# Kernel tuning notes

Measured on AMD Instinct MI355X. Metric: run time of the kernel, lower is better.

The kernel has to match this reference:

```python
import jax, jax.numpy as jnp
import numpy as np

EMBED_DIM = 1024
N_HEADS = 16

def setup_inputs() -> dict:
    key = jax.random.key(0)
    ks = jax.random.split(key, 5)
    C = EMBED_DIM
    std = 1.0 / np.sqrt(C)
    x = jax.random.normal(ks[0], (2, 2048, C), dtype=jnp.float32)
    w_attn = jax.random.normal(ks[1], (C, 3 * C), dtype=jnp.float32) * std  # (in, out)
    b_attn = jax.random.normal(ks[2], (3 * C,), dtype=jnp.float32) * 0.01
    w_proj = jax.random.normal(ks[3], (C, C), dtype=jnp.float32) * std
    b_proj = jax.random.normal(ks[4], (C,), dtype=jnp.float32) * 0.01
    return {"x": x, "w_attn": w_attn, "b_attn": b_attn, "w_proj": w_proj, "b_proj": b_proj}

def reference(x, w_attn, b_attn, w_proj, b_proj):
    B, T, C = x.shape
    H = N_HEADS
    D = C // H
    qkv = x @ w_attn + b_attn                      # (B, T, 3C)
    q, k, v = jnp.split(qkv, 3, axis=2)
    # (B, T, C) -> (B, H, T, D)
    q = q.reshape(B, T, H, D).transpose(0, 2, 1, 3)
    k = k.reshape(B, T, H, D).transpose(0, 2, 1, 3)
    v = v.reshape(B, T, H, D).transpose(0, 2, 1, 3)
    # Faithful to source: query is divided by scale BEFORE QK^T, and the
    # similarity is divided by scale AGAIN before softmax (net scale = 1/D).
    scale = jnp.asarray(D, dtype=x.dtype) ** 0.5
    q = q / scale
    sim = jnp.einsum('bhnd,bhsd->bhns', q, k)      # (B, H, T, T)
    causal = jnp.tril(jnp.ones((T, T), dtype=bool))
    neg_min = jnp.finfo(sim.dtype).min
    sim = jnp.where(causal[None, None, :, :], sim, neg_min)
    attn = jax.nn.softmax(sim / scale, axis=-1)
    out = jnp.einsum('bhns,bhsd->bhnd', attn, v)   # (B, H, T, D)
    # source: gqa returns (b n h d), forward does transpose(1,2) -> (b h n d)
    # then .view(B, T, C); net effect is reshaping the (B,H,T,D) layout.
    y = out.reshape(B, T, C)
    y = y @ w_proj + b_proj
    return y
```

## Files before the change

kernel.cpp:

```cpp
#include <hip/hip_runtime.h>
#include <hip/hip_bf16.h>

#define BB 2
#define TT 2048
#define CC 1024
#define HH 16
#define DD 64
#define MM (BB*TT)
#define QSZ ((size_t)MM*CC)

#define QSCALE 0.022542110013890053f

typedef __attribute__((ext_vector_type(8))) short bf16x8;
typedef __attribute__((ext_vector_type(4))) float f32x4;
typedef __attribute__((address_space(1))) const unsigned char as1_u8;
typedef __attribute__((address_space(3))) unsigned char as3_u8;

struct alignas(8) bf16x4_s { __hip_bfloat16 h[4]; };

static __device__ __forceinline__ unsigned cvt_pk_bf16(float lo, float hi) {
    unsigned r;
    asm("v_cvt_pk_bf16_f32 %0, %1, %2" : "=v"(r) : "v"(lo), "v"(hi));
    return r;
}

static __device__ __forceinline__ float fast_exp2(float x) {
    return __builtin_amdgcn_exp2f(x);
}

__constant__ unsigned char U_sqi[30] = {
    5,11,11,10,10,15,15, 4,9,9,13,14,14,14,15, 8,8,12,12,13,13,
    3,7,7,12, 6,6, 2,1,0};
__constant__ unsigned char U_t0[30] = {
    0,0,12,0,11,0,11, 0,0,10,0,0,10,20,22, 0,9,0,9,10,19,
    0,0,8,18, 0,7, 0,0,0};
__constant__ unsigned char U_t1[30] = {
    12,12,24,11,22,11,22, 10,10,20,10,10,20,30,32, 9,18,9,18,19,28,
    8,8,16,26, 7,14, 6,4,2};
__constant__ unsigned char U_pu[30] = {
    255,10,11,8,9,21,22, 255,6,7,15,18,19,20,23, 4,5,12,13,16,17,
    255,2,3,14, 0,1, 255,255,255};

__global__ __launch_bounds__(256) void prep_kernel(
    const float* __restrict__ x,  __hip_bfloat16* __restrict__ xb,
    const float* __restrict__ wa, __hip_bfloat16* __restrict__ wqkvT,
    const float* __restrict__ wp, __hip_bfloat16* __restrict__ wprojT)
{
    __shared__ float tile[64][68];
    const int t = threadIdx.x;
    const int b = blockIdx.x;
    if (b < 2048) {
        const int i = (b * 256 + t) * 8;
        const float4 a = *(const float4*)&x[i];
        const float4 c = *(const float4*)&x[i + 4];
        uint2 lo, hi;
        lo.x = cvt_pk_bf16(a.x, a.y); lo.y = cvt_pk_bf16(a.z, a.w);
        hi.x = cvt_pk_bf16(c.x, c.y); hi.y = cvt_pk_bf16(c.z, c.w);
        *(uint2*)&xb[i] = lo;
        *(uint2*)&xb[i + 4] = hi;
        return;
    }
    const float* in; __hip_bfloat16* outp; int R, Cc, bx, by;
    if (b < 2816) { const int i = b - 2048; in = wa; outp = wqkvT; R = CC; Cc = 3*CC; bx = i % 48; by = i / 48; }
    else          { const int i = b - 2816; in = wp; outp = wprojT; R = CC; Cc = CC;  bx = i % 16; by = i / 16; }
    const int c0 = bx * 64, r0 = by * 64;
    {
        const int r = t >> 2, cb = (t & 3) * 16;
        #pragma unroll
        for (int i = 0; i < 4; ++i)
            *(float4*)&tile[r][cb + i*4] = *(const float4*)&in[(size_t)(r0 + r)*Cc + c0 + cb + i*4];
    }
    __syncthreads();
    {
        const int c = t >> 2, rb = (t & 3) * 16;
        uint2 o0, o1;
        o0.x = cvt_pk_bf16(tile[rb+0][c],  tile[rb+1][c]);
        o0.y = cvt_pk_bf16(tile[rb+2][c],  tile[rb+3][c]);
        o1.x = cvt_pk_bf16(tile[rb+4][c],  tile[rb+5][c]);
        o1.y = cvt_pk_bf16(tile[rb+6][c],  tile[rb+7][c]);
        __hip_bfloat16* dst = outp + (size_t)(c0 + c)*R + r0 + rb;
        *(uint2*)&dst[0] = o0; *(uint2*)&dst[4] = o1;
        o0.x = cvt_pk_bf16(tile[rb+8][c],  tile[rb+9][c]);
        o0.y = cvt_pk_bf16(tile[rb+10][c], tile[rb+11][c]);
        o1.x = cvt_pk_bf16(tile[rb+12][c], tile[rb+13][c]);
        o1.y = cvt_pk_bf16(tile[rb+14][c], tile[rb+15][c]);
        *(uint2*)&dst[8] = o0; *(uint2*)&dst[12] = o1;
    }
}

template<int MODE>
__global__ __launch_bounds__(256) void gemm_mfma(
    const __hip_bfloat16* __restrict__ A,
    const __hip_bfloat16* __restrict__ BT,
    const float* __restrict__ bias,
    void* __restrict__ out, int M, int N, int K)
{
    __shared__ __hip_bfloat16 As[128][64];
    __shared__ __hip_bfloat16 Bs[128][64];

    const int tid = threadIdx.x;
    const int w = tid >> 6, l = tid & 63;
    const int lr = l & 15, lg = l >> 4;
    const int wr = w >> 1, wc = w & 1;
    const int rsw = (lr & 7) << 4;
    const int lsw = ((l & 7) ^ (l >> 3)) * 8;

    const int nwg = gridDim.x * gridDim.y;
    const int bid = blockIdx.y * gridDim.x + blockIdx.x;
    const int swz_id = (bid & 7) * (nwg >> 3) + (bid >> 3);
    const int row0 = (swz_id / gridDim.x) * 128;
    const int col0 = (swz_id % gridDim.x) * 128;

    f32x4 acc[4][4] = {};

    for (int k0 = 0; k0 < K; k0 += 64) {
        __syncthreads();
        #pragma unroll
        for (int i = 0; i < 4; ++i) {
            const int br = w*32 + i*8;
            const __hip_bfloat16* ga = A  + (size_t)(row0 + br + (l>>3))*K + k0 + lsw;
            __builtin_amdgcn_global_load_lds((as1_u8*)ga, (as3_u8*)&As[br][0], 16, 0, 0);
            const __hip_bfloat16* gb = BT + (size_t)(col0 + br + (l>>3))*K + k0 + lsw;
            __builtin_amdgcn_global_load_lds((as1_u8*)gb, (as3_u8*)&Bs[br][0], 16, 0, 0);
        }
        __syncthreads();

        #pragma unroll
        for (int s = 0; s < 2; ++s) {
            bf16x8 af[4], bfr[4];
            #pragma unroll
            for (int m = 0; m < 4; ++m) {
                const char* ab = (const char*)&As[wr*64 + m*16 + lr][0];
                af[m] = *(const bf16x8*)(ab + ((s*64 + lg*16) ^ rsw));
            }
            #pragma unroll
            for (int n = 0; n < 4; ++n) {
                const char* bb = (const char*)&Bs[wc*64 + n*16 + lr][0];
                bfr[n] = *(const bf16x8*)(bb + ((s*64 + lg*16) ^ rsw));
            }
            #pragma unroll
            for (int m = 0; m < 4; ++m)
                #pragma unroll
                for (int n = 0; n < 4; ++n)
                    acc[m][n] = __builtin_amdgcn_mfma_f32_16x16x32_bf16(af[m], bfr[n], acc[m][n], 0, 0, 0);
        }
    }

    #pragma unroll
    for (int m = 0; m < 4; ++m) {
        #pragma unroll
        for (int n = 0; n < 4; ++n) {
            const int ng = col0 + wc*64 + n*16 + lr;
            const float bv = bias[ng];
            const int mg0 = row0 + wr*64 + m*16 + lg*4;
            if (MODE == 0) {
                const int which = ng >> 10, c = ng & 1023;
                const int h = c >> 6, d = c & 63;
                if (which == 2) {
                    const int b = mg0 >> 11, t0 = mg0 & 2047;
                    uint2 pv;
                    pv.x = cvt_pk_bf16(acc[m][n][0] + bv, acc[m][n][1] + bv);
                    pv.y = cvt_pk_bf16(acc[m][n][2] + bv, acc[m][n][3] + bv);
                    *(uint2*)((__hip_bfloat16*)out + (size_t)2*QSZ +
                        (((size_t)(b*HH + h))*DD + d)*TT + t0) = pv;
                } else {
                    #pragma unroll
                    for (int r = 0; r < 4; ++r) {
                        const int mg = mg0 + r;
                        float v = acc[m][n][r] + bv;
                        if (which == 0) v *= QSCALE;
                        const int b = mg >> 11, t = mg & 2047;
                        ((__hip_bfloat16*)out)[(size_t)which*QSZ +
                            (((size_t)(b*HH + h))*TT + t)*DD + d] = __float2bfloat16(v);
                    }
                }
            } else {
                #pragma unroll
                for (int r = 0; r < 4; ++r)
                    ((float*)out)[(size_t)(mg0 + r)*N + ng] = acc[m][n][r] + bv;
            }
        }
    }
}

__global__ __launch_bounds__(512) void attn_mfma(
    const __hip_bfloat16* __restrict__ Qb,
    const __hip_bfloat16* __restrict__ Kb,
    const __hip_bfloat16* __restrict__ Vb,
    __hip_bfloat16* __restrict__ Ob,
    __hip_bfloat16* __restrict__ Opart,
    float* __restrict__ Lpart)
{
    __shared__ __hip_bfloat16 k_lds[64][64];
    __shared__ __hip_bfloat16 vT[64][64];
    __shared__ __hip_bfloat16 p_lds[8][16][64];

    const int tid = threadIdx.x;
    const int w  = tid >> 6;
    const int l  = tid & 63;
    const int lr = l & 15;
    const int lg = l >> 4;
    const int swz = (lr & 7) << 4;

    const int bid  = blockIdx.x;
    const int loc  = bid >> 3;
    const int bh   = (bid & 7) * 4 + (loc & 3);
    const int u    = loc >> 2;
    const int sqi  = U_sqi[u];
    const int t0i  = U_t0[u];
    const int t1i  = U_t1[u];
    const int pu   = U_pu[u];
    const int qb   = sqi * 128;

    const __hip_bfloat16* Qh = Qb + (size_t)bh*TT*DD;
    const __hip_bfloat16* Kh = Kb + (size_t)bh*TT*DD;
    const __hip_bfloat16* Vh = Vb + (size_t)bh*DD*TT;

    bf16x8 qa[2];
    const int qrow = qb + w*16 + lr;
    {
        const __hip_bfloat16* qp = Qh + (size_t)qrow*DD + lg*8;
        qa[0] = *(const bf16x8*)(qp);
        qa[1] = *(const bf16x8*)(qp + 32);
    }

    const int off0 = (16*lg) ^ swz;
    const int off1 = (64 + 16*lg) ^ swz;
    const char* kr0b = (const char*)&k_lds[lr][0];
    const char* vr0b = (const char*)&vT[lr][0];
    char* pwb = (char*)&p_lds[w][lr][0];
    int pwo[4];
    #pragma unroll
    for (int mt = 0; mt < 4; ++mt) pwo[mt] = (32*mt + 8*lg) ^ swz;

    const int sthalf = tid >> 8;
    const int stid = tid & 255;
    const int srow = stid >> 2, sch = stid & 3;
    const int wswz = (srow & 7) << 4;
    char* swr = sthalf ? (char*)&vT[srow][0] : (char*)&k_lds[srow][0];
    const int wo0 = (sch*32) ^ wswz, wo1 = (sch*32 + 16) ^ wswz;
    const __hip_bfloat16* ssrc = sthalf
        ? (Vh + (size_t)srow*TT + t0i*64 + sch*16)
        : (Kh + (size_t)(t0i*64 + srow)*DD + sch*16);
    const size_t sstride = sthalf ? 64 : (size_t)64*DD;

    float4 sr0 = *(const float4*)ssrc, sr1 = *(const float4*)(ssrc + 8);
    ssrc += sstride;
    *(float4*)(swr + wo0) = sr0; *(float4*)(swr + wo1) = sr1;
    __syncthreads();

    f32x4 oacc[4] = {};
    f32x4 lacc = {0.f, 0.f, 0.f, 0.f};

    for (int t = t0i; t < t1i; ++t) {
        const int kv0 = t * 64;
        const bool has_next = (t + 1 < t1i);

        if (has_next) {
            sr0 = *(const float4*)ssrc; sr1 = *(const float4*)(ssrc + 8);
            ssrc += sstride;
        }

        const bool dead = (w < 4) && (t == 2*sqi + 1);
        if (!dead) {
            f32x4 sacc[4] = {};
            __builtin_amdgcn_s_setprio(1);
            #pragma unroll
            for (int mt = 0; mt < 4; ++mt) {
                const bf16x8 kb0 = *(const bf16x8*)(kr0b + mt*2048 + off0);
                const bf16x8 kb1 = *(const bf16x8*)(kr0b + mt*2048 + off1);
                sacc[mt] = __builtin_amdgcn_mfma_f32_16x16x32_bf16(kb0, qa[0], sacc[mt], 0, 0, 0);
                sacc[mt] = __builtin_amdgcn_mfma_f32_16x16x32_bf16(kb1, qa[1], sacc[mt], 0, 0, 0);
            }
            __builtin_amdgcn_s_setprio(0);

            if (t >= 2*sqi) {
                #pragma unroll
                for (int mt = 0; mt < 4; ++mt)
                    #pragma unroll
                    for (int r = 0; r < 4; ++r)
                        if (kv0 + mt*16 + lg*4 + r > qrow) sacc[mt][r] = -3.0e38f;
            }
            #pragma unroll
            for (int mt = 0; mt < 4; ++mt) {
                const float p0 = fast_exp2(sacc[mt][0]), p1 = fast_exp2(sacc[mt][1]);
                const float p2 = fast_exp2(sacc[mt][2]), p3 = fast_exp2(sacc[mt][3]);
                lacc[mt] += (p0 + p1) + (p2 + p3);
                uint2 pp;
                pp.x = cvt_pk_bf16(p0, p1);
                pp.y = cvt_pk_bf16(p2, p3);
                *(uint2*)(pwb + pwo[mt]) = pp;
            }

            const bf16x8 pb0 = *(const bf16x8*)(pwb + off0);
            const bf16x8 pb1 = *(const bf16x8*)(pwb + off1);
            __builtin_amdgcn_s_setprio(1);
            #pragma unroll
            for (int dt = 0; dt < 4; ++dt) {
                const bf16x8 vb0 = *(const bf16x8*)(vr0b + dt*2048 + off0);
                const bf16x8 vb1 = *(const bf16x8*)(vr0b + dt*2048 + off1);
                oacc[dt] = __builtin_amdgcn_mfma_f32_16x16x32_bf16(vb0, pb0, oacc[dt], 0, 0, 0);
                oacc[dt] = __builtin_amdgcn_mfma_f32_16x16x32_bf16(vb1, pb1, oacc[dt], 0, 0, 0);
            }
            __builtin_amdgcn_s_setprio(0);
        }

        if (has_next) {
            __syncthreads();
            *(float4*)(swr + wo0) = sr0; *(float4*)(swr + wo1) = sr1;
            __syncthreads();
        }
    }

    float l_r = (lacc[0] + lacc[1]) + (lacc[2] + lacc[3]);
    l_r += __shfl_xor(l_r, 16);
    l_r += __shfl_xor(l_r, 32);

    if (pu != 255) {
        const int unit = bh*24 + pu;
        const int rowu = w*16 + lr;
        __hip_bfloat16* Oprow = Opart + ((size_t)unit*128 + rowu)*64;
        #pragma unroll
        for (int dt = 0; dt < 4; ++dt) {
            uint2 ov;
            ov.x = cvt_pk_bf16(oacc[dt][0], oacc[dt][1]);
            ov.y = cvt_pk_bf16(oacc[dt][2], oacc[dt][3]);
            *(uint2*)(Oprow + dt*16 + lg*4) = ov;
        }
        if (lg == 0) Lpart[unit*128 + rowu] = l_r;
    } else {
        __hip_bfloat16* Orow = Ob + ((size_t)bh*TT + qrow)*DD;
        const float inv = 1.0f / l_r;
        #pragma unroll
        for (int dt = 0; dt < 4; ++dt) {
            uint2 ov;
            ov.x = cvt_pk_bf16(oacc[dt][0]*inv, oacc[dt][1]*inv);
            ov.y = cvt_pk_bf16(oacc[dt][2]*inv, oacc[dt][3]*inv);
            *(uint2*)(Orow + dt*16 + lg*4) = ov;
        }
    }
}

__global__ __launch_bounds__(256) void attn_combine(
    const __hip_bfloat16* __restrict__ Opart,
    const float* __restrict__ Lpart,
    __hip_bfloat16* __restrict__ Ob)
{
    const int w = threadIdx.x >> 6, d = threadIdx.x & 63;
    const int rowg = blockIdx.x * 4 + w;
    const int bh  = rowg / 1280;
    const int rem = rowg - bh * 1280;
    const int spb = rem >> 7;
    const int r   = rem & 127;
    const int nu  = (spb < 6) ? 2 : 3;
    const int pu0 = bh*24 + ((spb < 6) ? 2*spb : 12 + 3*(spb - 6));
    float o = 0.f, lsum = 0.f;
    for (int i = 0; i < nu; ++i) {
        o    += __bfloat162float(Opart[((size_t)(pu0 + i)*128 + r)*64 + d]);
        lsum += Lpart[(pu0 + i)*128 + r];
    }
    const int qrow = (6 + spb)*128 + r;
    Ob[((size_t)bh*TT + qrow)*DD + d] = __float2bfloat16(o / lsum);
}

extern "C" void kernel_launch(void* const* d_in, const int* in_sizes, int n_in,
                              void* d_out, int out_size, void* d_ws, size_t ws_size,
                              hipStream_t stream)
{
    const float* x      = (const float*)d_in[0];
    const float* w_attn = (const float*)d_in[1];
    const float* b_attn = (const float*)d_in[2];
    const float* w_proj = (const float*)d_in[3];
    const float* b_proj = (const float*)d_in[4];
    float* out = (float*)d_out;

    __hip_bfloat16* xb     = (__hip_bfloat16*)d_ws;
    __hip_bfloat16* wqkvT  = xb + QSZ;
    __hip_bfloat16* wprojT = wqkvT + 3*CC*CC;
    __hip_bfloat16* Qb     = wprojT + CC*CC;
    __hip_bfloat16* Kb     = Qb + QSZ;
    __hip_bfloat16* Vt     = Kb + QSZ;
    __hip_bfloat16* Ob     = Vt + QSZ;

    __hip_bfloat16* Opart  = xb;
    float*          Lpart  = (float*)(xb + (size_t)768*128*64);

    prep_kernel<<<dim3(3072), 256, 0, stream>>>(x, xb, w_attn, wqkvT, w_proj, wprojT);

    gemm_mfma<0><<<dim3(3*CC/128, MM/128), 256, 0, stream>>>(xb, wqkvT, b_attn, (void*)Qb, MM, 3*CC, CC);

    attn_mfma<<<dim3(960), 512, 0, stream>>>(Qb, Kb, Vt, Ob, Opart, Lpart);

    attn_combine<<<dim3(40960/4), 256, 0, stream>>>(Opart, Lpart, Ob);

    gemm_mfma<1><<<dim3(CC/128, MM/128), 256, 0, stream>>>(Ob, wprojT, b_proj, (void*)out, MM, CC, CC);
}
```

Measured before the change: 105.6 us.

## Replace QKV GEMM with 256x256-tile double-buffered global-to-LDS kernel

Splits the templated GEMM into a dedicated QKV kernel and a projection kernel. The QKV kernel uses 256x256 output tiles with 512 threads and 128KB of dynamic LDS. It double-buffers K-slices via direct global_load_lds with vmcnt-based waits and raises wave priority around the MFMA block. The aim is better operand reuse and latency hiding, but the grid shrinks to 192 workgroups, which may leave CUs idle on a 256-CU part.

```diff
diff --git a/kernel.cpp b/kernel.cpp
--- a/kernel.cpp
+++ b/kernel.cpp
@@ -88,12 +88,124 @@
     }
 }
 
-template<int MODE>
-__global__ __launch_bounds__(256) void gemm_mfma(
+__global__ __launch_bounds__(512, 2) void gemm_qkv256(
     const __hip_bfloat16* __restrict__ A,
     const __hip_bfloat16* __restrict__ BT,
     const float* __restrict__ bias,
-    void* __restrict__ out, int M, int N, int K)
+    __hip_bfloat16* __restrict__ out, int M, int N, int K)
+{
+    extern __shared__ char smem[];
+    char* AsB = smem;
+    char* BsB = smem + 65536;
+
+    const int tid = threadIdx.x;
+    const int w = tid >> 6, l = tid & 63;
+    const int lr = l & 15, lg = l >> 4;
+    const int wm = w >> 2, wn = w & 3;
+    const int rsw = (lr & 7) << 4;
+    const int lsw = ((l & 7) ^ (l >> 3)) * 8;
+
+    const int nwg = gridDim.x * gridDim.y;
+    const int bid = blockIdx.y * gridDim.x + blockIdx.x;
+    const int swz_id = (bid & 7) * (nwg >> 3) + (bid >> 3);
+    const int row0 = (swz_id / gridDim.x) * 256;
+    const int col0 = (swz_id % gridDim.x) * 256;
+
+    const __hip_bfloat16* gA = A  + (size_t)(row0 + (l >> 3))*K + lsw;
+    const __hip_bfloat16* gB = BT + (size_t)(col0 + (l >> 3))*K + lsw;
+
+    f32x4 acc[8][4] = {};
+    const int nt = K >> 6;
+
+    #pragma unroll
+    for (int ttp = 0; ttp < 2; ++ttp) {
+        #pragma unroll
+        for (int i = 0; i < 4; ++i) {
+            const int br = w*32 + i*8;
+            __builtin_amdgcn_global_load_lds((as1_u8*)(gA + (size_t)br*K + ttp*64),
+                (as3_u8*)(AsB + ttp*32768 + br*128), 16, 0, 0);
+            __builtin_amdgcn_global_load_lds((as1_u8*)(gB + (size_t)br*K + ttp*64),
+                (as3_u8*)(BsB + ttp*32768 + br*128), 16, 0, 0);
+        }
+    }
+
+    for (int t = 0; t < nt; ++t) {
+        if (t == nt - 1) asm volatile("s_waitcnt vmcnt(0)" ::: "memory");
+        else             asm volatile("s_waitcnt vmcnt(8)" ::: "memory");
+        __builtin_amdgcn_s_barrier();
+
+        const int c = t & 1;
+        const char* aB = AsB + c*32768;
+        const char* bB = BsB + c*32768;
+        #pragma unroll
+        for (int s = 0; s < 2; ++s) {
+            bf16x8 af[8], bfr[4];
+            #pragma unroll
+            for (int mf = 0; mf < 8; ++mf)
+                af[mf] = *(const bf16x8*)(aB + (wm*128 + mf*16 + lr)*128 + ((s*64 + lg*16) ^ rsw));
+            #pragma unroll
+            for (int nf = 0; nf < 4; ++nf)
+                bfr[nf] = *(const bf16x8*)(bB + (wn*64 + nf*16 + lr)*128 + ((s*64 + lg*16) ^ rsw));
+            __builtin_amdgcn_s_setprio(1);
+            #pragma unroll
+            for (int mf = 0; mf < 8; ++mf)
+                #pragma unroll
+                for (int nf = 0; nf < 4; ++nf)
+                    acc[mf][nf] = __builtin_amdgcn_mfma_f32_16x16x32_bf16(af[mf], bfr[nf], acc[mf][nf], 0, 0, 0);
+            __builtin_amdgcn_s_setprio(0);
+        }
+
+        __builtin_amdgcn_s_barrier();
+
+        if (t + 2 < nt) {
+            const int kk = (t + 2) * 64;
+            #pragma unroll
+            for (int i = 0; i < 4; ++i) {
+                const int br = w*32 + i*8;
+                __builtin_amdgcn_global_load_lds((as1_u8*)(gA + (size_t)br*K + kk),
+                    (as3_u8*)(AsB + c*32768 + br*128), 16, 0, 0);
+                __builtin_amdgcn_global_load_lds((as1_u8*)(gB + (size_t)br*K + kk),
+                    (as3_u8*)(BsB + c*32768 + br*128), 16, 0, 0);
+            }
+        }
+    }
+
+    #pragma unroll
+    for (int mf = 0; mf < 8; ++mf) {
+        #pragma unroll
+        for (int nf = 0; nf < 4; ++nf) {
+            const int ng = col0 + wn*64 + nf*16 + lr;
+            const float bv = bias[ng];
+            const int mg0 = row0 + wm*128 + mf*16 + lg*4;
+            const int which = ng >> 10, cq = ng & 1023;
+            const int h = cq >> 6, d = cq & 63;
+            if (which == 2) {
+                const int b = mg0 >> 11, t0 = mg0 & 2047;
+                uint2 pv;
+                pv.x = cvt_pk_bf16(acc[mf][nf][0] + bv, acc[mf][nf][1] + bv);
+                pv.y = cvt_pk_bf16(acc[mf][nf][2] + bv, acc[mf][nf][3] + bv);
+                *(uint2*)(out + (size_t)2*QSZ +
+                    (((size_t)(b*HH + h))*DD + d)*TT + t0) = pv;
+            } else {
+                #pragma unroll
+                for (int r = 0; r < 4; ++r) {
+                    const int mg = mg0 + r;
+                    float v = acc[mf][nf][r] + bv;
+                    if (which == 0) v *= QSCALE;
+                    const int b = mg >> 11, t = mg & 2047;
+                    out[(size_t)which*QSZ +
+                        (((size_t)(b*HH + h))*TT + t)*DD + d] = __float2bfloat16(v);
+                }
+            }
+        }
+    }
+}
+
+__global__ __launch_bounds__(256) void gemm_proj(
+    const __hip_bfloat16* __restrict__ A,
+    const __hip_bfloat16* __restrict__ BT,
+    const float* __restrict__ bias,
+    float* __restrict__ out, int M, int N, int K)
 {
     __shared__ __hip_bfloat16 As[128][64];
     __shared__ __hip_bfloat16 Bs[128][64];
@@ -153,32 +265,9 @@
             const int ng = col0 + wc*64 + n*16 + lr;
             const float bv = bias[ng];
             const int mg0 = row0 + wr*64 + m*16 + lg*4;
-            if (MODE == 0) {
-                const int which = ng >> 10, c = ng & 1023;
-                const int h = c >> 6, d = c & 63;
-                if (which == 2) {
-                    const int b = mg0 >> 11, t0 = mg0 & 2047;
-                    uint2 pv;
-                    pv.x = cvt_pk_bf16(acc[m][n][0] + bv, acc[m][n][1] + bv);
-                    pv.y = cvt_pk_bf16(acc[m][n][2] + bv, acc[m][n][3] + bv);
-                    *(uint2*)((__hip_bfloat16*)out + (size_t)2*QSZ +
-                        (((size_t)(b*HH + h))*DD + d)*TT + t0) = pv;
-                } else {
-                    #pragma unroll
-                    for (int r = 0; r < 4; ++r) {
-                        const int mg = mg0 + r;
-                        float v = acc[m][n][r] + bv;
-                        if (which == 0) v *= QSCALE;
-                        const int b = mg >> 11, t = mg & 2047;
-                        ((__hip_bfloat16*)out)[(size_t)which*QSZ +
-                            (((size_t)(b*HH + h))*TT + t)*DD + d] = __float2bfloat16(v);
-                    }
-                }
-            } else {
-                #pragma unroll
-                for (int r = 0; r < 4; ++r)
-                    ((float*)out)[(size_t)(mg0 + r)*N + ng] = acc[m][n][r] + bv;
-            }
+            #pragma unroll
+            for (int r = 0; r < 4; ++r)
+                out[(size_t)(mg0 + r)*N + ng] = acc[m][n][r] + bv;
         }
     }
 }
@@ -385,13 +474,17 @@
     __hip_bfloat16* Opart  = xb;
     float*          Lpart  = (float*)(xb + (size_t)768*128*64);
 
+    (void)hipFuncSetAttribute((const void*)gemm_qkv256,
+        hipFuncAttributeMaxDynamicSharedMemorySize, 131072);
+
     prep_kernel<<<dim3(3072), 256, 0, stream>>>(x, xb, w_attn, wqkvT, w_proj, wprojT);
 
-    gemm_mfma<0><<<dim3(3*CC/128, MM/128), 256, 0, stream>>>(xb, wqkvT, b_attn, (void*)Qb, MM, 3*CC, CC);
+    gemm_qkv256<<<dim3(3*CC/256, MM/256), 512, 131072, stream>>>(
+        xb, wqkvT, b_attn, Qb, MM, 3*CC, CC);
 
     attn_mfma<<<dim3(960), 512, 0, stream>>>(Qb, Kb, Vt, Ob, Opart, Lpart);
 
     attn_combine<<<dim3(40960/4), 256, 0, stream>>>(Opart, Lpart, Ob);
 
-    gemm_mfma<1><<<dim3(CC/128, MM/128), 256, 0, stream>>>(Ob, wprojT, b_proj, (void*)out, MM, CC, CC);
-}
+    gemm_proj<<<dim3(CC/128, MM/128), 256, 0, stream>>>(Ob, wprojT, b_proj, out, MM, CC, CC);
+}
```

Result: slower. 110.3 us (+4.4%).

## Refine split-KV work partition for causal attention into 40 units per head

Applied to the files above, without the earlier changes.

Replaces the 30-unit per-head causal attention schedule with a 40-unit schedule in which query blocks from 4 onward are split across 2, 3 or 4 KV-range partial units, giving 1280 blocks instead of 960. The combine kernel is updated to merge the new partition counts, and partial outputs now spill into a second workspace segment past Ob. The aim is better load balance and CU occupancy across the attention grid. The cost is more partial writes and more combine traffic.

```diff
diff --git a/kernel.cpp b/kernel.cpp
--- a/kernel.cpp
+++ b/kernel.cpp
@@ -28,18 +28,28 @@
     return __builtin_amdgcn_exp2f(x);
 }
 
-__constant__ unsigned char U_sqi[30] = {
-    5,11,11,10,10,15,15, 4,9,9,13,14,14,14,15, 8,8,12,12,13,13,
-    3,7,7,12, 6,6, 2,1,0};
-__constant__ unsigned char U_t0[30] = {
-    0,0,12,0,11,0,11, 0,0,10,0,0,10,20,22, 0,9,0,9,10,19,
-    0,0,8,18, 0,7, 0,0,0};
-__constant__ unsigned char U_t1[30] = {
-    12,12,24,11,22,11,22, 10,10,20,10,10,20,30,32, 9,18,9,18,19,28,
-    8,8,16,26, 7,14, 6,4,2};
-__constant__ unsigned char U_pu[30] = {
-    255,10,11,8,9,21,22, 255,6,7,15,18,19,20,23, 4,5,12,13,16,17,
-    255,2,3,14, 0,1, 255,255,255};
+__constant__ unsigned char U_sqi[40] = {
+    3,7,7,10,11,11,11,14,14,15,15,15,15,
+    6,6,9,9,10,10,12,12,13,13,13,13,14,14,
+    2,5,5,8,8,8,9,12,12, 4,4, 1, 0};
+__constant__ unsigned char U_t0[40] = {
+    0,0,8,0,0,8,16,0,8,0,8,16,24,
+    0,7,0,7,8,15,0,7,0,7,14,21,16,23,
+    0,0,6,0,6,12,14,14,20, 0,5, 0, 0};
+__constant__ unsigned char U_t1[40] = {
+    8,8,16,8,8,16,24,8,16,8,16,24,32,
+    7,14,7,14,15,22,7,14,7,14,21,28,23,30,
+    6,6,12,6,12,18,20,20,26, 5,10, 4, 2};
+__constant__ unsigned char U_pu[40] = {
+    255,6,7,14,17,18,19,28,29,32,33,34,35,
+    4,5,11,12,15,16,20,21,24,25,26,27,30,31,
+    255,2,3,8,9,10,13,22,23, 0,1, 255, 255};
+
+static __device__ __forceinline__ __hip_bfloat16* opart_base(
+    __hip_bfloat16* segA, __hip_bfloat16* segB, int unit) {
+    return (unit < 768) ? (segA + (size_t)unit * 8192)
+                        : (segB + (size_t)(unit - 768) * 8192);
+}
 
 __global__ __launch_bounds__(256) void prep_kernel(
     const float* __restrict__ x,  __hip_bfloat16* __restrict__ xb,
@@ -188,7 +198,8 @@
     const __hip_bfloat16* __restrict__ Kb,
     const __hip_bfloat16* __restrict__ Vb,
     __hip_bfloat16* __restrict__ Ob,
-    __hip_bfloat16* __restrict__ Opart,
+    __hip_bfloat16* __restrict__ OpA,
+    __hip_bfloat16* __restrict__ OpB,
     float* __restrict__ Lpart)
 {
     __shared__ __hip_bfloat16 k_lds[64][64];
@@ -317,9 +328,9 @@
     l_r += __shfl_xor(l_r, 32);
 
     if (pu != 255) {
-        const int unit = bh*24 + pu;
+        const int unit = bh*36 + pu;
         const int rowu = w*16 + lr;
-        __hip_bfloat16* Oprow = Opart + ((size_t)unit*128 + rowu)*64;
+        __hip_bfloat16* Oprow = opart_base(OpA, OpB, unit) + (size_t)rowu*64;
         #pragma unroll
         for (int dt = 0; dt < 4; ++dt) {
             uint2 ov;
@@ -342,24 +353,32 @@
 }
 
 __global__ __launch_bounds__(256) void attn_combine(
-    const __hip_bfloat16* __restrict__ Opart,
+    const __hip_bfloat16* __restrict__ OpA,
+    const __hip_bfloat16* __restrict__ OpB,
     const float* __restrict__ Lpart,
     __hip_bfloat16* __restrict__ Ob)
 {
     const int w = threadIdx.x >> 6, d = threadIdx.x & 63;
     const int rowg = blockIdx.x * 4 + w;
-    const int bh  = rowg / 1280;
-    const int rem = rowg - bh * 1280;
+    const int bh  = rowg / 1536;
+    const int rem = rowg - bh * 1536;
     const int spb = rem >> 7;
     const int r   = rem & 127;
-    const int nu  = (spb < 6) ? 2 : 3;
-    const int pu0 = bh*24 + ((spb < 6) ? 2*spb : 12 + 3*(spb - 6));
+    int nu, pu0;
+    if (spb < 4)      { nu = 2; pu0 = 2*spb; }
+    else if (spb < 8) { nu = 3; pu0 = 8 + 3*(spb - 4); }
+    else              { nu = 4; pu0 = 20 + 4*(spb - 8); }
+    const int unit0 = bh*36 + pu0;
     float o = 0.f, lsum = 0.f;
     for (int i = 0; i < nu; ++i) {
-        o    += __bfloat162float(Opart[((size_t)(pu0 + i)*128 + r)*64 + d]);
-        lsum += Lpart[(pu0 + i)*128 + r];
-    }
-    const int qrow = (6 + spb)*128 + r;
+        const int unit = unit0 + i;
+        const __hip_bfloat16* base = (unit < 768)
+            ? (OpA + (size_t)unit * 8192)
+            : (OpB + (size_t)(unit - 768) * 8192);
+        o    += __bfloat162float(base[(size_t)r*64 + d]);
+        lsum += Lpart[unit*128 + r];
+    }
+    const int qrow = (4 + spb)*128 + r;
     Ob[((size_t)bh*TT + qrow)*DD + d] = __float2bfloat16(o / lsum);
 }
 
@@ -382,16 +401,17 @@
     __hip_bfloat16* Vt     = Kb + QSZ;
     __hip_bfloat16* Ob     = Vt + QSZ;
 
-    __hip_bfloat16* Opart  = xb;
-    float*          Lpart  = (float*)(xb + (size_t)768*128*64);
+    __hip_bfloat16* OpA   = xb;
+    float*          Lpart = (float*)(xb + (size_t)768*8192);
+    __hip_bfloat16* OpB   = Ob + QSZ;
 
     prep_kernel<<<dim3(3072), 256, 0, stream>>>(x, xb, w_attn, wqkvT, w_proj, wprojT);
 
     gemm_mfma<0><<<dim3(3*CC/128, MM/128), 256, 0, stream>>>(xb, wqkvT, b_attn, (void*)Qb, MM, 3*CC, CC);
 
-    attn_mfma<<<dim3(960), 512, 0, stream>>>(Qb, Kb, Vt, Ob, Opart, Lpart);
-
-    attn_combine<<<dim3(40960/4), 256, 0, stream>>>(Opart, Lpart, Ob);
+    attn_mfma<<<dim3(1280), 512, 0, stream>>>(Qb, Kb, Vt, Ob, OpA, OpB, Lpart);
+
+    attn_combine<<<dim3(49152/4), 256, 0, stream>>>(OpA, OpB, Lpart, Ob);
 
     gemm_mfma<1><<<dim3(CC/128, MM/128), 256, 0, stream>>>(Ob, wprojT, b_proj, (void*)out, MM, CC, CC);
 }
```

Result: slower. 109.3 us (+3.5%).
